# Performance work log

Hardware: AMD Instinct MI355X
Metric: run time of the kernel (lower is better)

Reference implementation:

```python
import jax, jax.numpy as jnp
import numpy as np

EMBED = 128
HEADS = 8
HDIM = EMBED // HEADS  # 16
LN_EPS = 1e-5


def _angle_decay():
    # angle: 1/10000**linspace(0,1,HDIM//2), each value repeated twice -> (HDIM,)
    a = 1.0 / 10000 ** jnp.linspace(0.0, 1.0, HDIM // 2)
    angle = jnp.repeat(a, 2)
    # decay: log(1 - 2^(-initial_value - heads_range*h/H)), initial_value=1, heads_range=3
    h = jnp.arange(HEADS, dtype=jnp.float32)
    decay = jnp.log1p(-jnp.exp2(-(1.0 + 3.0 * h / HEADS)))
    return angle, decay


def _rotary(t, sin, cos):
    # t: (..., S, D); sin/cos: (S, D)
    return t * cos + jnp.concatenate([-t[..., 1::2], t[..., ::2]], axis=-1) * sin


def _layer_norm(x, g, b):
    mu = jnp.mean(x, axis=-1, keepdims=True)
    var = jnp.mean((x - mu) ** 2, axis=-1, keepdims=True)
    return (x - mu) * jax.lax.rsqrt(var + LN_EPS) * g + b


def setup_inputs() -> dict:
    key = jax.random.key(0)
    ks = jax.random.split(key, 6)
    B, N, C = 32, 8192, EMBED
    s = 0.02
    return {
        "x": jax.random.normal(ks[0], (B, N, C), dtype=jnp.float32),
        "wq": jax.random.normal(ks[1], (C, C), dtype=jnp.float32) * s,
        "bq": jnp.zeros((C,), jnp.float32),
        "wk": jax.random.normal(ks[2], (C, C), dtype=jnp.float32) * s,
        "bk": jnp.zeros((C,), jnp.float32),
        "wv": jax.random.normal(ks[3], (C, C), dtype=jnp.float32) * s,
        "bv": jnp.zeros((C,), jnp.float32),
        "ln1_g": jnp.ones((C,), jnp.float32),
        "ln1_b": jnp.zeros((C,), jnp.float32),
        "ffn_w1": jax.random.normal(ks[4], (C, 4 * C), dtype=jnp.float32) * s,
        "ffn_b1": jnp.zeros((4 * C,), jnp.float32),
        "ffn_w2": jax.random.normal(ks[5], (4 * C, C), dtype=jnp.float32) * s,
        "ffn_b2": jnp.zeros((C,), jnp.float32),
        "ln2_g": jnp.ones((C,), jnp.float32),
        "ln2_b": jnp.zeros((C,), jnp.float32),
    }


def reference(x, wq, bq, wk, bk, wv, bv, ln1_g, ln1_b,
              ffn_w1, ffn_b1, ffn_w2, ffn_b2, ln2_g, ln2_b):
    B, N, C = x.shape  # attention runs over B (frames), per location N
    xt = jnp.transpose(x, (1, 0, 2))  # (N, B, C)
    S = B  # seq_len for pos encoder

    angle, decay = _angle_decay()
    idx = jnp.arange(S, dtype=jnp.float32)
    sin = jnp.sin(idx[:, None] * angle[None, :])  # (S, HDIM)
    cos = jnp.cos(idx[:, None] * angle[None, :])
    # decay mask: |i - j| * decay_h -> (H, S, S)
    dist = jnp.abs(idx[:, None] - idx[None, :])
    mask = dist[None, :, :] * decay[:, None, None]

    def proj(w, b):
        t = xt @ w + b  # (N, S, C)
        return jnp.transpose(t.reshape(N, S, HEADS, HDIM), (2, 0, 1, 3))  # (H, N, S, D)

    q = _rotary(proj(wq, bq), sin, cos)
    k = _rotary(proj(wk, bk), sin, cos)
    v = proj(wv, bv)

    scores = jnp.einsum('hnqd,hnkd->hnqk', q, k) + mask[:, None, :, :]
    attn = jax.nn.softmax(scores, axis=-1)  # dropout is identity in eval
    out = jnp.einsum('hnqk,hnkd->hnqd', attn, v)  # (H, N, S, D)
    out = jnp.transpose(out, (1, 2, 0, 3)).reshape(N, S, C)

    out = _layer_norm(out + xt, ln1_g, ln1_b)
    ffn = jax.nn.relu(out @ ffn_w1 + ffn_b1) @ ffn_w2 + ffn_b2
    out = _layer_norm(ffn + out, ln2_g, ln2_b)
    return jnp.transpose(out, (1, 0, 2))  # (B, N, C)
```

## Files before the change

### kernel.cpp

```cpp
#include <hip/hip_runtime.h>


#define NN 8192
#define BS 32
#define CC 128
#define HH 8
#define DD 16
#define FF 512
#define QS 129

typedef __attribute__((ext_vector_type(8))) short bf16x8;
typedef __attribute__((ext_vector_type(4))) float f32x4;
typedef __attribute__((ext_vector_type(4))) unsigned int u32x4;
typedef __attribute__((ext_vector_type(2))) unsigned int u32x2;

#define XB_H 0
#define QB_H 4352
#define KB_H 8704
#define VT_H 13056
#define P_H 17152
#define P_HEAD 1152
#define P_STR 36
#define TAB_F 8576
#define O1B_H 4352
#define H_H 8704
#define O2_H 0
#define LDS_BYTES 52736

__device__ inline unsigned short f2bf(float f) {
  unsigned u = __builtin_bit_cast(unsigned, f);
  u = (u + 0x7FFFu + ((u >> 16) & 1u)) >> 16;
  return (unsigned short)u;
}
__device__ inline float bf2f(unsigned short h) {
  unsigned u = ((unsigned)h) << 16;
  return __builtin_bit_cast(float, u);
}

__global__ void pack_weights(const float* __restrict__ wq, const float* __restrict__ wk,
                             const float* __restrict__ wv, const float* __restrict__ w1,
                             const float* __restrict__ w2, unsigned short* __restrict__ outp)
{
  const int id = blockIdx.x * 256 + threadIdx.x;
  if (id >= 23040) return;
  if (id >= 22528) {
    const int i = id - 22528;
    const int s = i >> 4, d = i & 15;
    const float a = exp2f(-1.89824462565f * (float)(d >> 1));
    const float ang = (float)s * a;
    float2* tab = (float2*)(outp + 180224);
    tab[i] = make_float2(sinf(ang), cosf(ang));
    return;
  }
  const int l = id & 63;
  const int chunk = id >> 6;
  const float* W; int ldw, colbase, k0;
  if (chunk < 96) {
    const int ct = chunk >> 2, kk = chunk & 3;
    W = (ct < 8) ? wq : (ct < 16) ? wk : wv;
    ldw = CC; colbase = (ct & 7) * 16 + (l & 15); k0 = kk * 32 + (l >> 4) * 8;
  } else if (chunk < 224) {
    const int c2 = chunk - 96, ct = c2 >> 2, kk = c2 & 3;
    W = w1; ldw = FF; colbase = ct * 16 + (l & 15); k0 = kk * 32 + (l >> 4) * 8;
  } else {
    const int c2 = chunk - 224, ct = c2 >> 4, kk = c2 & 15;
    W = w2; ldw = CC; colbase = ct * 16 + (l & 15); k0 = kk * 32 + (l >> 4) * 8;
  }
  unsigned int o[4];
  #pragma unroll
  for (int jj = 0; jj < 4; ++jj) {
    const unsigned lo = f2bf(W[(size_t)(k0 + 2 * jj) * ldw + colbase]);
    const unsigned hi = f2bf(W[(size_t)(k0 + 2 * jj + 1) * ldw + colbase]);
    o[jj] = lo | (hi << 16);
  }
  *(u32x4*)(outp + (size_t)id * 8) = (u32x4){o[0], o[1], o[2], o[3]};
}

__global__ __launch_bounds__(512, 6) void fused_mfma(
    const float* __restrict__ x,
    const float* __restrict__ bq, const float* __restrict__ bk, const float* __restrict__ bv,
    const float* __restrict__ ln1g, const float* __restrict__ ln1b,
    const float* __restrict__ b1, const float* __restrict__ b2,
    const float* __restrict__ ln2g, const float* __restrict__ ln2b,
    const unsigned short* __restrict__ wpack,
    const float2* __restrict__ rott,
    float* __restrict__ out)
{
  extern __shared__ char smem[];
  float* ldsf = (float*)smem;
  unsigned short* ldsh = (unsigned short*)smem;
  const int n = blockIdx.x;
  const int t = threadIdx.x;
  const int w = t >> 6;
  const int l = t & 63;
  const int lr = l & 15;
  const int lg = l >> 4;

  {
    const int s = t >> 4, c0 = (t & 15) * 8;
    const float* xp = x + ((size_t)s * NN + n) * CC + c0;
    const float4 v0 = *(const float4*)xp;
    const float4 v1 = *(const float4*)(xp + 4);
    u32x4 pk;
    pk[0] = (unsigned)f2bf(v0.x) | ((unsigned)f2bf(v0.y) << 16);
    pk[1] = (unsigned)f2bf(v0.z) | ((unsigned)f2bf(v0.w) << 16);
    pk[2] = (unsigned)f2bf(v1.x) | ((unsigned)f2bf(v1.y) << 16);
    pk[3] = (unsigned)f2bf(v1.z) | ((unsigned)f2bf(v1.w) << 16);
    *(u32x4*)(ldsh + XB_H + s * 136 + c0) = pk;
    ((float2*)(ldsf + TAB_F))[t] = rott[t];
  }
  __syncthreads();

  {
    f32x4 acc[2][3];
    #pragma unroll
    for (int c = 0; c < 3; ++c) {
      const int ct = 3 * w + c;
      const int col = (ct & 7) * 16 + lr;
      const float* bb = (ct < 8) ? bq : (ct < 16) ? bk : bv;
      const float b = bb[col];
      acc[0][c] = (f32x4){b, b, b, b};
      acc[1][c] = acc[0][c];
    }
    #pragma unroll
    for (int kk = 0; kk < 4; ++kk) {
      const bf16x8 a0 = *(const bf16x8*)(ldsh + XB_H + lr * 136 + kk * 32 + lg * 8);
      const bf16x8 a1 = *(const bf16x8*)(ldsh + XB_H + (16 + lr) * 136 + kk * 32 + lg * 8);
      #pragma unroll
      for (int c = 0; c < 3; ++c) {
        const int ct = 3 * w + c;
        const bf16x8 b = *(const bf16x8*)(wpack + ((size_t)(ct * 4 + kk) * 64 + l) * 8);
        acc[0][c] = __builtin_amdgcn_mfma_f32_16x16x32_bf16(a0, b, acc[0][c], 0, 0, 0);
        acc[1][c] = __builtin_amdgcn_mfma_f32_16x16x32_bf16(a1, b, acc[1][c], 0, 0, 0);
      }
    }
    float sn[2][4], cs[2][4];
    if (3 * w < 16) {
      #pragma unroll
      for (int rt = 0; rt < 2; ++rt)
        #pragma unroll
        for (int e = 0; e < 4; ++e) {
          const int row = rt * 16 + lg * 4 + e;
          const float2 tc = ((const float2*)(ldsf + TAB_F))[row * 16 + lr];
          sn[rt][e] = tc.x;
          cs[rt][e] = tc.y;
        }
    }
    const int pd = (lr < 8) ? (2 * lr + 1) : (2 * lr - 16);
    const float sgn = (lr < 8) ? -1.0f : 1.0f;
    const int psrc = (l & 48) | pd;
    #pragma unroll
    for (int c = 0; c < 3; ++c) {
      const int ct = 3 * w + c;
      if (ct < 16) {
        const int dst = (ct < 8) ? QB_H : KB_H;
        const int colbase = (ct & 7) * 16;
        #pragma unroll
        for (int rt = 0; rt < 2; ++rt)
          #pragma unroll
          for (int e = 0; e < 4; ++e) {
            const float v = acc[rt][c][e];
            const float pv = __shfl(v, psrc);
            const float r = v * cs[rt][e] + sgn * pv * sn[rt][e];
            ldsh[dst + (rt * 16 + lg * 4 + e) * 136 + colbase + lr] = f2bf(r);
          }
      } else {
        const int hv = ct - 16;
        #pragma unroll
        for (int rt = 0; rt < 2; ++rt)
          #pragma unroll
          for (int e = 0; e < 4; ++e)
            ldsh[VT_H + hv * 512 + lr * 32 + rt * 16 + lg * 4 + e] = f2bf(acc[rt][c][e]);
      }
    }
  }
  __syncthreads();

  {
    const int h16 = w * 16;
    const float dec = log1pf(-exp2f(-(1.0f + 0.375f * (float)w)));
    const bf16x8 z = {};
    bf16x8 Ak[2], Bq[2];
    #pragma unroll
    for (int kt = 0; kt < 2; ++kt)
      Ak[kt] = (lg < 2) ? *(const bf16x8*)(ldsh + KB_H + (kt * 16 + lr) * 136 + h16 + lg * 8) : z;
    #pragma unroll
    for (int qt = 0; qt < 2; ++qt)
      Bq[qt] = (lg < 2) ? *(const bf16x8*)(ldsh + QB_H + (qt * 16 + lr) * 136 + h16 + lg * 8) : z;
    f32x4 accs[2][2];
    #pragma unroll
    for (int kt = 0; kt < 2; ++kt)
      #pragma unroll
      for (int qt = 0; qt < 2; ++qt) {
        #pragma unroll
        for (int e = 0; e < 4; ++e) {
          const int q = qt * 16 + lr;
          const int k = kt * 16 + lg * 4 + e;
          accs[kt][qt][e] = fabsf((float)(q - k)) * dec;
        }
        accs[kt][qt] = __builtin_amdgcn_mfma_f32_16x16x32_bf16(Ak[kt], Bq[qt], accs[kt][qt], 0, 0, 0);
      }
    unsigned short* Pl = ldsh + P_H + w * P_HEAD;
    #pragma unroll
    for (int qt = 0; qt < 2; ++qt) {
      float mx = accs[0][qt][0];
      #pragma unroll
      for (int kt = 0; kt < 2; ++kt)
        #pragma unroll
        for (int e = 0; e < 4; ++e) mx = fmaxf(mx, accs[kt][qt][e]);
      mx = fmaxf(mx, __shfl_xor(mx, 16));
      mx = fmaxf(mx, __shfl_xor(mx, 32));
      float p[2][4];
      float sm = 0.0f;
      #pragma unroll
      for (int kt = 0; kt < 2; ++kt)
        #pragma unroll
        for (int e = 0; e < 4; ++e) { p[kt][e] = __expf(accs[kt][qt][e] - mx); sm += p[kt][e]; }
      sm += __shfl_xor(sm, 16);
      sm += __shfl_xor(sm, 32);
      const float inv = 1.0f / sm;
      #pragma unroll
      for (int kt = 0; kt < 2; ++kt) {
        u32x2 pw;
        pw[0] = (unsigned)f2bf(p[kt][0] * inv) | ((unsigned)f2bf(p[kt][1] * inv) << 16);
        pw[1] = (unsigned)f2bf(p[kt][2] * inv) | ((unsigned)f2bf(p[kt][3] * inv) << 16);
        *(u32x2*)(Pl + (qt * 16 + lr) * P_STR + kt * 16 + lg * 4) = pw;
      }
    }
    const bf16x8 Bv = *(const bf16x8*)(ldsh + VT_H + w * 512 + lr * 32 + lg * 8);
    #pragma unroll
    for (int qt = 0; qt < 2; ++qt) {
      const bf16x8 Ap = *(const bf16x8*)(Pl + (qt * 16 + lr) * P_STR + lg * 8);
      f32x4 z4 = {0.0f, 0.0f, 0.0f, 0.0f};
      const f32x4 o = __builtin_amdgcn_mfma_f32_16x16x32_bf16(Ap, Bv, z4, 0, 0, 0);
      #pragma unroll
      for (int e = 0; e < 4; ++e)
        ldsh[QB_H + (qt * 16 + lg * 4 + e) * 136 + h16 + lr] = f2bf(o[e]);
    }
  }
  __syncthreads();

  {
    const int row = t >> 4, sub = t & 15;
    const unsigned short* Or = ldsh + QB_H + row * 136 + sub * 8;
    const unsigned short* Xr = ldsh + XB_H + row * 136 + sub * 8;
    float v[8];
    #pragma unroll
    for (int i = 0; i < 8; ++i) v[i] = bf2f(Or[i]) + bf2f(Xr[i]);
    float sum = 0.0f;
    #pragma unroll
    for (int i = 0; i < 8; ++i) sum += v[i];
    #pragma unroll
    for (int m = 1; m < 16; m <<= 1) sum += __shfl_xor(sum, m);
    const float mu = sum * (1.0f / 128.0f);
    float s2 = 0.0f;
    #pragma unroll
    for (int i = 0; i < 8; ++i) { const float d = v[i] - mu; s2 += d * d; }
    #pragma unroll
    for (int m = 1; m < 16; m <<= 1) s2 += __shfl_xor(s2, m);
    const float rstd = rsqrtf(s2 * (1.0f / 128.0f) + 1e-5f);
    u32x4 pk;
    #pragma unroll
    for (int i = 0; i < 4; ++i) {
      const int c = sub * 8 + 2 * i;
      const float e0 = (v[2 * i] - mu) * rstd * ln1g[c] + ln1b[c];
      const float e1 = (v[2 * i + 1] - mu) * rstd * ln1g[c + 1] + ln1b[c + 1];
      pk[i] = (unsigned)f2bf(e0) | ((unsigned)f2bf(e1) << 16);
    }
    *(u32x4*)(ldsh + O1B_H + row * 136 + sub * 8) = pk;
  }
  __syncthreads();

  {
    f32x4 acc1[2][4];
    #pragma unroll
    for (int c = 0; c < 4; ++c) {
      const float b = b1[(4 * w + c) * 16 + lr];
      acc1[0][c] = (f32x4){b, b, b, b};
      acc1[1][c] = acc1[0][c];
    }
    #pragma unroll
    for (int kk = 0; kk < 4; ++kk) {
      const bf16x8 a0 = *(const bf16x8*)(ldsh + O1B_H + lr * 136 + kk * 32 + lg * 8);
      const bf16x8 a1 = *(const bf16x8*)(ldsh + O1B_H + (16 + lr) * 136 + kk * 32 + lg * 8);
      #pragma unroll
      for (int c = 0; c < 4; ++c) {
        const int chunk = 96 + (4 * w + c) * 4 + kk;
        const bf16x8 b = *(const bf16x8*)(wpack + ((size_t)chunk * 64 + l) * 8);
        acc1[0][c] = __builtin_amdgcn_mfma_f32_16x16x32_bf16(a0, b, acc1[0][c], 0, 0, 0);
        acc1[1][c] = __builtin_amdgcn_mfma_f32_16x16x32_bf16(a1, b, acc1[1][c], 0, 0, 0);
      }
    }
    #pragma unroll
    for (int p = 0; p < 2; ++p)
      #pragma unroll
      for (int c = 0; c < 4; ++c) {
        const int col = (4 * w + c) * 16 + lr;
        #pragma unroll
        for (int e = 0; e < 4; ++e)
          ldsh[H_H + (p * 16 + lg * 4 + e) * 552 + col] = f2bf(fmaxf(acc1[p][c][e], 0.0f));
      }
  }
  __syncthreads();

  {
    const int col = w * 16 + lr;
    const float b = b2[col];
    f32x4 acc2[2];
    acc2[0] = (f32x4){b, b, b, b};
    acc2[1] = acc2[0];
    #pragma unroll
    for (int kk = 0; kk < 16; ++kk) {
      const bf16x8 a0 = *(const bf16x8*)(ldsh + H_H + lr * 552 + kk * 32 + lg * 8);
      const bf16x8 a1 = *(const bf16x8*)(ldsh + H_H + (16 + lr) * 552 + kk * 32 + lg * 8);
      const int chunk = 224 + w * 16 + kk;
      const bf16x8 bb = *(const bf16x8*)(wpack + ((size_t)chunk * 64 + l) * 8);
      acc2[0] = __builtin_amdgcn_mfma_f32_16x16x32_bf16(a0, bb, acc2[0], 0, 0, 0);
      acc2[1] = __builtin_amdgcn_mfma_f32_16x16x32_bf16(a1, bb, acc2[1], 0, 0, 0);
    }
    #pragma unroll
    for (int p = 0; p < 2; ++p)
      #pragma unroll
      for (int e = 0; e < 4; ++e) {
        const int srow = p * 16 + lg * 4 + e;
        const float res = bf2f(ldsh[O1B_H + srow * 136 + col]);
        ldsh[O2_H + srow * 136 + col] = f2bf(acc2[p][e] + res);
      }
  }
  __syncthreads();

  {
    const int row = t >> 4, sub = t & 15;
    const unsigned short* Or = ldsh + O2_H + row * 136 + sub * 8;
    float v[8];
    #pragma unroll
    for (int i = 0; i < 8; ++i) v[i] = bf2f(Or[i]);
    float sum = 0.0f;
    #pragma unroll
    for (int i = 0; i < 8; ++i) sum += v[i];
    #pragma unroll
    for (int m = 1; m < 16; m <<= 1) sum += __shfl_xor(sum, m);
    const float mu = sum * (1.0f / 128.0f);
    float s2 = 0.0f;
    #pragma unroll
    for (int i = 0; i < 8; ++i) { const float d = v[i] - mu; s2 += d * d; }
    #pragma unroll
    for (int m = 1; m < 16; m <<= 1) s2 += __shfl_xor(s2, m);
    const float rstd = rsqrtf(s2 * (1.0f / 128.0f) + 1e-5f);
    const int c0 = sub * 8;
    float4 r0, r1;
    r0.x = (v[0] - mu) * rstd * ln2g[c0 + 0] + ln2b[c0 + 0];
    r0.y = (v[1] - mu) * rstd * ln2g[c0 + 1] + ln2b[c0 + 1];
    r0.z = (v[2] - mu) * rstd * ln2g[c0 + 2] + ln2b[c0 + 2];
    r0.w = (v[3] - mu) * rstd * ln2g[c0 + 3] + ln2b[c0 + 3];
    r1.x = (v[4] - mu) * rstd * ln2g[c0 + 4] + ln2b[c0 + 4];
    r1.y = (v[5] - mu) * rstd * ln2g[c0 + 5] + ln2b[c0 + 5];
    r1.z = (v[6] - mu) * rstd * ln2g[c0 + 6] + ln2b[c0 + 6];
    r1.w = (v[7] - mu) * rstd * ln2g[c0 + 7] + ln2b[c0 + 7];
    float* op = out + ((size_t)row * NN + n) * CC + c0;
    *(float4*)op = r0;
    *(float4*)(op + 4) = r1;
  }
}

__global__ __launch_bounds__(512, 4) void fused_retention_block(
    const float* __restrict__ x,
    const float* __restrict__ wq, const float* __restrict__ bq,
    const float* __restrict__ wk, const float* __restrict__ bk,
    const float* __restrict__ wv, const float* __restrict__ bv,
    const float* __restrict__ ln1g, const float* __restrict__ ln1b,
    const float* __restrict__ w1, const float* __restrict__ b1,
    const float* __restrict__ w2, const float* __restrict__ b2,
    const float* __restrict__ ln2g, const float* __restrict__ ln2b,
    float* __restrict__ out)
{
  const int n = blockIdx.x;
  const int t = threadIdx.x;
  __shared__ float SM[3 * BS * QS];
  float* Qs = SM;
  float* Ks = SM + BS * QS;
  float* Vs = SM + 2 * BS * QS;
  {
    const int o4 = t & 31;
    const int sp = t >> 5;
    const float* xr0 = x + ((size_t)(2 * sp) * NN + n) * CC;
    const float* xr1 = xr0 + (size_t)NN * CC;
    for (int m = 0; m < 3; ++m) {
      const float* W  = (m == 0) ? wq : (m == 1) ? wk : wv;
      const float* bb = (m == 0) ? bq : (m == 1) ? bk : bv;
      float* O = SM + m * BS * QS;
      float b4[4];
      *(float4*)b4 = *(const float4*)(bb + o4 * 4);
      float a0[4] = {b4[0], b4[1], b4[2], b4[3]};
      float a1[4] = {b4[0], b4[1], b4[2], b4[3]};
      for (int c4 = 0; c4 < 32; ++c4) {
        float xa4[4], xb4[4];
        *(float4*)xa4 = *(const float4*)(xr0 + c4 * 4);
        *(float4*)xb4 = *(const float4*)(xr1 + c4 * 4);
        const float* wp = W + (c4 * 4) * CC + o4 * 4;
        #pragma unroll
        for (int j = 0; j < 4; ++j) {
          float w4[4];
          *(float4*)w4 = *(const float4*)(wp + j * CC);
          #pragma unroll
          for (int e = 0; e < 4; ++e) { a0[e] += xa4[j] * w4[e]; a1[e] += xb4[j] * w4[e]; }
        }
      }
      float* q0 = O + (2 * sp) * QS + o4 * 4;
      float* q1 = O + (2 * sp + 1) * QS + o4 * 4;
      #pragma unroll
      for (int e = 0; e < 4; ++e) { q0[e] = a0[e]; q1[e] = a1[e]; }
    }
  }
  __syncthreads();
  {
    const int tt = t & 255;
    const int s = tt >> 3;
    const int h = tt & 7;
    float* row = ((t < 256) ? Qs : Ks) + s * QS + h * DD;
    float v[DD];
    #pragma unroll
    for (int d = 0; d < DD; ++d) v[d] = row[d];
    #pragma unroll
    for (int d = 0; d < DD; ++d) {
      const int j = d >> 1;
      const float a = exp2f(-1.89824462565f * (float)j);
      const float ang = (float)s * a;
      const float sn = sinf(ang);
      const float cs = cosf(ang);
      const float rot = (d < 8) ? -v[2 * d + 1] : v[2 * (d - 8)];
      row[d] = v[d] * cs + rot * sn;
    }
  }
  __syncthreads();
  if (t < 256) {
    const int h = t >> 5;
    const int qi = t & 31;
    const float dec = log1pf(-exp2f(-(1.0f + 0.375f * (float)h)));
    float q[DD];
    const float* Qr = Qs + qi * QS + h * DD;
    #pragma unroll
    for (int d = 0; d < DD; ++d) q[d] = Qr[d];
    float sc[BS];
    float mx = -3.0e38f;
    #pragma unroll
    for (int jj = 0; jj < BS; ++jj) {
      const float* Kr = Ks + jj * QS + h * DD;
      float acc = fabsf((float)(qi - jj)) * dec;
      #pragma unroll
      for (int d = 0; d < DD; ++d) acc += q[d] * Kr[d];
      sc[jj] = acc;
      mx = fmaxf(mx, acc);
    }
    float sum = 0.0f;
    #pragma unroll
    for (int jj = 0; jj < BS; ++jj) { const float p = __expf(sc[jj] - mx); sc[jj] = p; sum += p; }
    const float inv = 1.0f / sum;
    float o[DD];
    #pragma unroll
    for (int d = 0; d < DD; ++d) o[d] = 0.0f;
    #pragma unroll
    for (int jj = 0; jj < BS; ++jj) {
      const float p = sc[jj] * inv;
      const float* Vr = Vs + jj * QS + h * DD;
      #pragma unroll
      for (int d = 0; d < DD; ++d) o[d] += p * Vr[d];
    }
    float* Od = Qs + qi * QS + h * DD;
    #pragma unroll
    for (int d = 0; d < DD; ++d) Od[d] = o[d];
  }
  __syncthreads();
  {
    const int row = t >> 4;
    const int sub = t & 15;
    float* Orow = Qs + row * QS + sub * 8;
    const float* xrow = x + ((size_t)row * NN + n) * CC + sub * 8;
    float v[8];
    #pragma unroll
    for (int i = 0; i < 8; ++i) v[i] = Orow[i] + xrow[i];
    float sum = 0.0f;
    #pragma unroll
    for (int i = 0; i < 8; ++i) sum += v[i];
    #pragma unroll
    for (int m = 1; m < 16; m <<= 1) sum += __shfl_xor(sum, m);
    const float mu = sum * (1.0f / 128.0f);
    float s2 = 0.0f;
    #pragma unroll
    for (int i = 0; i < 8; ++i) { const float d = v[i] - mu; s2 += d * d; }
    #pragma unroll
    for (int m = 1; m < 16; m <<= 1) s2 += __shfl_xor(s2, m);
    const float rstd = rsqrtf(s2 * (1.0f / 128.0f) + 1e-5f);
    #pragma unroll
    for (int i = 0; i < 8; ++i) {
      const int c = sub * 8 + i;
      Orow[i] = (v[i] - mu) * rstd * ln1g[c] + ln1b[c];
    }
  }
  __syncthreads();
  float* Hb = Ks;
  const int f4  = t & 127;
  const int sb4 = (t >> 7) * 4;
  const int o4f = t & 31;
  const int sF  = t >> 5;
  for (int p = 0; p < 2; ++p) {
    {
      float acc[4][4];
      float b14[4];
      *(float4*)b14 = *(const float4*)(b1 + f4 * 4);
      #pragma unroll
      for (int i = 0; i < 4; ++i)
        #pragma unroll
        for (int e = 0; e < 4; ++e) acc[i][e] = b14[e];
      const float* O1b = Qs + (p * 16 + sb4) * QS;
      for (int c = 0; c < CC; ++c) {
        float w4[4];
        *(float4*)w4 = *(const float4*)(w1 + c * FF + f4 * 4);
        #pragma unroll
        for (int i = 0; i < 4; ++i) {
          const float xv = O1b[i * QS + c];
          #pragma unroll
          for (int e = 0; e < 4; ++e) acc[i][e] += xv * w4[e];
        }
      }
      #pragma unroll
      for (int i = 0; i < 4; ++i) {
        float4 r;
        r.x = fmaxf(acc[i][0], 0.0f); r.y = fmaxf(acc[i][1], 0.0f);
        r.z = fmaxf(acc[i][2], 0.0f); r.w = fmaxf(acc[i][3], 0.0f);
        *(float4*)(Hb + (sb4 + i) * FF + f4 * 4) = r;
      }
    }
    __syncthreads();
    {
      const int s = p * 16 + sF;
      float acc[4];
      *(float4*)acc = *(const float4*)(b2 + o4f * 4);
      const float* hrow = Hb + sF * FF;
      for (int k = 0; k < FF; ++k) {
        const float hv = hrow[k];
        float w4[4];
        *(float4*)w4 = *(const float4*)(w2 + k * CC + o4f * 4);
        #pragma unroll
        for (int e = 0; e < 4; ++e) acc[e] += hv * w4[e];
      }
      const float* res = Qs + s * QS + o4f * 4;
      #pragma unroll
      for (int e = 0; e < 4; ++e) acc[e] += res[e];
      float sum = acc[0] + acc[1] + acc[2] + acc[3];
      #pragma unroll
      for (int m = 1; m < 32; m <<= 1) sum += __shfl_xor(sum, m);
      const float mu = sum * (1.0f / 128.0f);
      float s2 = 0.0f;
      #pragma unroll
      for (int e = 0; e < 4; ++e) { const float d = acc[e] - mu; s2 += d * d; }
      #pragma unroll
      for (int m = 1; m < 32; m <<= 1) s2 += __shfl_xor(s2, m);
      const float rstd = rsqrtf(s2 * (1.0f / 128.0f) + 1e-5f);
      float4 r;
      const int c0 = o4f * 4;
      r.x = (acc[0] - mu) * rstd * ln2g[c0 + 0] + ln2b[c0 + 0];
      r.y = (acc[1] - mu) * rstd * ln2g[c0 + 1] + ln2b[c0 + 1];
      r.z = (acc[2] - mu) * rstd * ln2g[c0 + 2] + ln2b[c0 + 2];
      r.w = (acc[3] - mu) * rstd * ln2g[c0 + 3] + ln2b[c0 + 3];
      *(float4*)(out + ((size_t)s * NN + n) * CC + c0) = r;
    }
    __syncthreads();
  }
}

extern "C" void kernel_launch(void* const* d_in, const int* in_sizes, int n_in,
                              void* d_out, int out_size, void* d_ws, size_t ws_size,
                              hipStream_t stream) {
  (void)in_sizes; (void)n_in; (void)out_size;
  const float* x    = (const float*)d_in[0];
  const float* wq   = (const float*)d_in[1];
  const float* bq_  = (const float*)d_in[2];
  const float* wk   = (const float*)d_in[3];
  const float* bk_  = (const float*)d_in[4];
  const float* wv   = (const float*)d_in[5];
  const float* bv_  = (const float*)d_in[6];
  const float* ln1g = (const float*)d_in[7];
  const float* ln1b = (const float*)d_in[8];
  const float* w1   = (const float*)d_in[9];
  const float* b1   = (const float*)d_in[10];
  const float* w2   = (const float*)d_in[11];
  const float* b2   = (const float*)d_in[12];
  const float* ln2g = (const float*)d_in[13];
  const float* ln2b = (const float*)d_in[14];
  float* outp = (float*)d_out;

  if (ws_size >= (size_t)364544) {
    unsigned short* wpack = (unsigned short*)d_ws;
    const float2* rott = (const float2*)((const char*)d_ws + 360448);
    pack_weights<<<90, 256, 0, stream>>>(wq, wk, wv, w1, w2, wpack);
    fused_mfma<<<NN, 512, LDS_BYTES, stream>>>(
        x, bq_, bk_, bv_, ln1g, ln1b, b1, b2, ln2g, ln2b, wpack, rott, outp);
  } else {
    fused_retention_block<<<NN, 512, 0, stream>>>(
        x, wq, bq_, wk, bk_, wv, bv_, ln1g, ln1b,
        w1, b1, w2, b2, ln2g, ln2b, outp);
  }
}
```

Baseline: 214.5 us.

## Shrink LDS footprint via buffer aliasing and XOR swizzle to raise occupancy

Reorganizes the shared-memory plan so buffers alias one another: P reuses the Q region, O1/H/O2 reuse the X region, and the FFN activations use an unpadded XOR-swizzled layout. This cuts LDS from about 52.7KB to 40KB per block so more blocks can be resident per CU. Two extra barriers are added to keep the aliased regions safe. f2bf is switched to the HIP bf16 intrinsic and the V-transpose stride is padded.

```diff
diff --git a/kernel.cpp b/kernel.cpp
--- a/kernel.cpp
+++ b/kernel.cpp
@@ -1,4 +1,5 @@
 #include <hip/hip_runtime.h>
+#include <hip/hip_bf16.h>
 
 
 #define NN 8192
@@ -18,19 +19,20 @@
 #define QB_H 4352
 #define KB_H 8704
 #define VT_H 13056
-#define P_H 17152
+#define TAB_F 8832
+#define P_H 4352
 #define P_HEAD 1152
 #define P_STR 36
-#define TAB_F 8576
-#define O1B_H 4352
-#define H_H 8704
-#define O2_H 0
-#define LDS_BYTES 52736
+#define O_H 13568
+#define O1B_H 0
+#define H_H 4096
+#define LDS_BYTES 40960
 
 __device__ inline unsigned short f2bf(float f) {
-  unsigned u = __builtin_bit_cast(unsigned, f);
-  u = (u + 0x7FFFu + ((u >> 16) & 1u)) >> 16;
-  return (unsigned short)u;
+  return __builtin_bit_cast(unsigned short, __float2bfloat16(f));
+}
+__device__ inline unsigned pk2bf(float lo, float hi) {
+  return (unsigned)f2bf(lo) | ((unsigned)f2bf(hi) << 16);
 }
 __device__ inline float bf2f(unsigned short h) {
   unsigned u = ((unsigned)h) << 16;
@@ -68,11 +70,9 @@
   }
   unsigned int o[4];
   #pragma unroll
-  for (int jj = 0; jj < 4; ++jj) {
-    const unsigned lo = f2bf(W[(size_t)(k0 + 2 * jj) * ldw + colbase]);
-    const unsigned hi = f2bf(W[(size_t)(k0 + 2 * jj + 1) * ldw + colbase]);
-    o[jj] = lo | (hi << 16);
-  }
+  for (int jj = 0; jj < 4; ++jj)
+    o[jj] = pk2bf(W[(size_t)(k0 + 2 * jj) * ldw + colbase],
+                  W[(size_t)(k0 + 2 * jj + 1) * ldw + colbase]);
   *(u32x4*)(outp + (size_t)id * 8) = (u32x4){o[0], o[1], o[2], o[3]};
 }
 
@@ -102,10 +102,10 @@
     const float4 v0 = *(const float4*)xp;
     const float4 v1 = *(const float4*)(xp + 4);
     u32x4 pk;
-    pk[0] = (unsigned)f2bf(v0.x) | ((unsigned)f2bf(v0.y) << 16);
-    pk[1] = (unsigned)f2bf(v0.z) | ((unsigned)f2bf(v0.w) << 16);
-    pk[2] = (unsigned)f2bf(v1.x) | ((unsigned)f2bf(v1.y) << 16);
-    pk[3] = (unsigned)f2bf(v1.z) | ((unsigned)f2bf(v1.w) << 16);
+    pk[0] = pk2bf(v0.x, v0.y);
+    pk[1] = pk2bf(v0.z, v0.w);
+    pk[2] = pk2bf(v1.x, v1.y);
+    pk[3] = pk2bf(v1.z, v1.w);
     *(u32x4*)(ldsh + XB_H + s * 136 + c0) = pk;
     ((float2*)(ldsf + TAB_F))[t] = rott[t];
   }
@@ -170,7 +170,7 @@
         for (int rt = 0; rt < 2; ++rt)
           #pragma unroll
           for (int e = 0; e < 4; ++e)
-            ldsh[VT_H + hv * 512 + lr * 32 + rt * 16 + lg * 4 + e] = f2bf(acc[rt][c][e]);
+            ldsh[VT_H + hv * 576 + lr * 36 + rt * 16 + lg * 4 + e] = f2bf(acc[rt][c][e]);
       }
     }
   }
@@ -187,6 +187,9 @@
     #pragma unroll
     for (int qt = 0; qt < 2; ++qt)
       Bq[qt] = (lg < 2) ? *(const bf16x8*)(ldsh + QB_H + (qt * 16 + lr) * 136 + h16 + lg * 8) : z;
+    const bf16x8 Bv = *(const bf16x8*)(ldsh + VT_H + w * 576 + lr * 36 + lg * 8);
+    __syncthreads();
+
     f32x4 accs[2][2];
     #pragma unroll
     for (int kt = 0; kt < 2; ++kt)
@@ -222,12 +225,11 @@
       #pragma unroll
       for (int kt = 0; kt < 2; ++kt) {
         u32x2 pw;
-        pw[0] = (unsigned)f2bf(p[kt][0] * inv) | ((unsigned)f2bf(p[kt][1] * inv) << 16);
-        pw[1] = (unsigned)f2bf(p[kt][2] * inv) | ((unsigned)f2bf(p[kt][3] * inv) << 16);
+        pw[0] = pk2bf(p[kt][0] * inv, p[kt][1] * inv);
+        pw[1] = pk2bf(p[kt][2] * inv, p[kt][3] * inv);
         *(u32x2*)(Pl + (qt * 16 + lr) * P_STR + kt * 16 + lg * 4) = pw;
       }
     }
-    const bf16x8 Bv = *(const bf16x8*)(ldsh + VT_H + w * 512 + lr * 32 + lg * 8);
     #pragma unroll
     for (int qt = 0; qt < 2; ++qt) {
       const bf16x8 Ap = *(const bf16x8*)(Pl + (qt * 16 + lr) * P_STR + lg * 8);
@@ -235,14 +237,14 @@
       const f32x4 o = __builtin_amdgcn_mfma_f32_16x16x32_bf16(Ap, Bv, z4, 0, 0, 0);
       #pragma unroll
       for (int e = 0; e < 4; ++e)
-        ldsh[QB_H + (qt * 16 + lg * 4 + e) * 136 + h16 + lr] = f2bf(o[e]);
+        ldsh[O_H + (qt * 16 + lg * 4 + e) * 136 + h16 + lr] = f2bf(o[e]);
     }
   }
   __syncthreads();
 
   {
     const int row = t >> 4, sub = t & 15;
-    const unsigned short* Or = ldsh + QB_H + row * 136 + sub * 8;
+    const unsigned short* Or = ldsh + O_H + row * 136 + sub * 8;
     const unsigned short* Xr = ldsh + XB_H + row * 136 + sub * 8;
     float v[8];
     #pragma unroll
@@ -263,11 +265,11 @@
     #pragma unroll
     for (int i = 0; i < 4; ++i) {
       const int c = sub * 8 + 2 * i;
-      const float e0 = (v[2 * i] - mu) * rstd * ln1g[c] + ln1b[c];
-      const float e1 = (v[2 * i + 1] - mu) * rstd * ln1g[c + 1] + ln1b[c + 1];
-      pk[i] = (unsigned)f2bf(e0) | ((unsigned)f2bf(e1) << 16);
-    }
-    *(u32x4*)(ldsh + O1B_H + row * 136 + sub * 8) = pk;
+      pk[i] = pk2bf((v[2 * i] - mu) * rstd * ln1g[c] + ln1b[c],
+                    (v[2 * i + 1] - mu) * rstd * ln1g[c + 1] + ln1b[c + 1]);
+    }
+    __syncthreads();
+    *(u32x4*)(ldsh + O1B_H + row * 128 + ((sub * 8) ^ ((row & 7) << 3))) = pk;
   }
   __syncthreads();
 
@@ -281,8 +283,9 @@
     }
     #pragma unroll
     for (int kk = 0; kk < 4; ++kk) {
-      const bf16x8 a0 = *(const bf16x8*)(ldsh + O1B_H + lr * 136 + kk * 32 + lg * 8);
-      const bf16x8 a1 = *(const bf16x8*)(ldsh + O1B_H + (16 + lr) * 136 + kk * 32 + lg * 8);
+      const int csw = (kk * 32 + lg * 8) ^ ((lr & 7) << 3);
+      const bf16x8 a0 = *(const bf16x8*)(ldsh + O1B_H + lr * 128 + csw);
+      const bf16x8 a1 = *(const bf16x8*)(ldsh + O1B_H + (16 + lr) * 128 + csw);
       #pragma unroll
       for (int c = 0; c < 4; ++c) {
         const int chunk = 96 + (4 * w + c) * 4 + kk;
@@ -297,8 +300,10 @@
       for (int c = 0; c < 4; ++c) {
         const int col = (4 * w + c) * 16 + lr;
         #pragma unroll
-        for (int e = 0; e < 4; ++e)
-          ldsh[H_H + (p * 16 + lg * 4 + e) * 552 + col] = f2bf(fmaxf(acc1[p][c][e], 0.0f));
+        for (int e = 0; e < 4; ++e) {
+          const int row = p * 16 + lg * 4 + e;
+          ldsh[H_H + row * 512 + (col ^ ((row & 7) << 3))] = f2bf(fmaxf(acc1[p][c][e], 0.0f));
+        }
       }
   }
   __syncthreads();
@@ -311,8 +316,9 @@
     acc2[1] = acc2[0];
     #pragma unroll
     for (int kk = 0; kk < 16; ++kk) {
-      const bf16x8 a0 = *(const bf16x8*)(ldsh + H_H + lr * 552 + kk * 32 + lg * 8);
-      const bf16x8 a1 = *(const bf16x8*)(ldsh + H_H + (16 + lr) * 552 + kk * 32 + lg * 8);
+      const int csw = (kk * 32 + lg * 8) ^ ((lr & 7) << 3);
+      const bf16x8 a0 = *(const bf16x8*)(ldsh + H_H + lr * 512 + csw);
+      const bf16x8 a1 = *(const bf16x8*)(ldsh + H_H + (16 + lr) * 512 + csw);
       const int chunk = 224 + w * 16 + kk;
       const bf16x8 bb = *(const bf16x8*)(wpack + ((size_t)chunk * 64 + l) * 8);
       acc2[0] = __builtin_amdgcn_mfma_f32_16x16x32_bf16(a0, bb, acc2[0], 0, 0, 0);
@@ -323,15 +329,16 @@
       #pragma unroll
       for (int e = 0; e < 4; ++e) {
         const int srow = p * 16 + lg * 4 + e;
-        const float res = bf2f(ldsh[O1B_H + srow * 136 + col]);
-        ldsh[O2_H + srow * 136 + col] = f2bf(acc2[p][e] + res);
+        const int idx = O1B_H + srow * 128 + (col ^ ((srow & 7) << 3));
+        const float res = bf2f(ldsh[idx]);
+        ldsh[idx] = f2bf(acc2[p][e] + res);
       }
   }
   __syncthreads();
 
   {
     const int row = t >> 4, sub = t & 15;
-    const unsigned short* Or = ldsh + O2_H + row * 136 + sub * 8;
+    const unsigned short* Or = ldsh + O1B_H + row * 128 + ((sub * 8) ^ ((row & 7) << 3));
     float v[8];
     #pragma unroll
     for (int i = 0; i < 8; ++i) v[i] = bf2f(Or[i]);
```

Measured after the change: 225.9 us. 5.3% more time.
